# Kernel optimization log

Measured on AMD Instinct MI355X. Metric: run time of the kernel, lower is better.

The kernel has to match this reference:

```python
import jax, jax.numpy as jnp
import numpy as np

DIM = 384; HEADS = 12; WS = 7; SHIFT = 3
IMG_H = 56; IMG_W = 56; B = 32; MLP_HID = 1536
N = WS * WS; HEAD_DIM = DIM // HEADS


def _rel_pos_index():
    # standard Swin relative position index, shape [N, N], values in [0, (2*WS-1)^2)
    coords = np.stack(np.meshgrid(np.arange(WS), np.arange(WS), indexing='ij')).reshape(2, -1)
    rel = (coords[:, :, None] - coords[:, None, :]).transpose(1, 2, 0)
    rel[..., 0] += WS - 1
    rel[..., 1] += WS - 1
    rel[..., 0] *= 2 * WS - 1
    return jnp.asarray(rel.sum(-1))

REL_IDX = _rel_pos_index()


def _shift_mask():
    # Swin shifted-window attention mask: 0 within region, -100 across regions
    img = np.zeros((IMG_H, IMG_W))
    cnt = 0
    for hs in (slice(0, -WS), slice(-WS, -SHIFT), slice(-SHIFT, None)):
        for ws_ in (slice(0, -WS), slice(-WS, -SHIFT), slice(-SHIFT, None)):
            img[hs, ws_] = cnt
            cnt += 1
    mw = img.reshape(IMG_H // WS, WS, IMG_W // WS, WS).transpose(0, 2, 1, 3).reshape(-1, N)
    am = mw[:, None, :] - mw[:, :, None]
    return jnp.asarray(np.where(am != 0, -100.0, 0.0).astype(np.float32))


def setup_inputs() -> dict:
    key = jax.random.key(0)
    ks = jax.random.split(key, 8)
    rn = lambda k, s: jax.random.normal(k, s, jnp.float32) * 0.02
    return {
        'x': jax.random.normal(ks[0], (B, IMG_H * IMG_W, DIM), jnp.float32),
        'mask': _shift_mask(),
        'w_ln1': jnp.ones((DIM,), jnp.float32), 'b_ln1': jnp.zeros((DIM,), jnp.float32),
        'w_qkv': rn(ks[1], (3 * DIM, DIM)), 'b_qkv': jnp.zeros((3 * DIM,), jnp.float32),
        'rel_bias': rn(ks[2], ((2 * WS - 1) ** 2, HEADS)),
        'w_proj': rn(ks[3], (DIM, DIM)), 'b_proj': jnp.zeros((DIM,), jnp.float32),
        'w_ln2': jnp.ones((DIM,), jnp.float32), 'b_ln2': jnp.zeros((DIM,), jnp.float32),
        'w_fc1': rn(ks[4], (MLP_HID, DIM)), 'b_fc1': jnp.zeros((MLP_HID,), jnp.float32),
        'w_fc2': rn(ks[5], (DIM, MLP_HID)), 'b_fc2': jnp.zeros((DIM,), jnp.float32),
        'H': IMG_H, 'W': IMG_W,
    }


def _ln(x, g, b, eps=1e-5):
    mu = x.mean(-1, keepdims=True)
    var = ((x - mu) ** 2).mean(-1, keepdims=True)
    return (x - mu) * jax.lax.rsqrt(var + eps) * g + b


def reference(x, mask, w_ln1, b_ln1, w_qkv, b_qkv, rel_bias, w_proj, b_proj,
              w_ln2, b_ln2, w_fc1, b_fc1, w_fc2, b_fc2, H, W):
    Bsz, L, C = x.shape
    nW = (H // WS) * (W // WS)
    shortcut = x
    h = _ln(x, w_ln1, b_ln1).reshape(Bsz, H, W, C)
    # cyclic shift
    h = jnp.roll(h, (-SHIFT, -SHIFT), axis=(1, 2))
    # window partition -> [B*nW, N, C]
    h = h.reshape(Bsz, H // WS, WS, W // WS, WS, C).transpose(0, 1, 3, 2, 4, 5).reshape(-1, N, C)
    nB = h.shape[0]
    qkv = (h @ w_qkv.T + b_qkv).reshape(nB, N, 3, HEADS, HEAD_DIM).transpose(2, 0, 3, 1, 4)
    q, k, v = qkv[0] * (HEAD_DIM ** -0.5), qkv[1], qkv[2]  # each [nB, heads, N, hd]
    attn = jnp.einsum('bhnd,bhmd->bhnm', q, k)
    bias = rel_bias[REL_IDX].transpose(2, 0, 1)  # [heads, N, N]
    attn = attn + bias[None]
    attn = attn.reshape(Bsz, nW, HEADS, N, N) + mask[None, :, None]
    attn = jax.nn.softmax(attn, axis=-1).reshape(nB, HEADS, N, N)
    o = jnp.einsum('bhnm,bhmd->bhnd', attn, v).transpose(0, 2, 1, 3).reshape(nB, N, C)
    o = o @ w_proj.T + b_proj
    # window reverse
    o = o.reshape(Bsz, H // WS, W // WS, WS, WS, C).transpose(0, 1, 3, 2, 4, 5).reshape(Bsz, H, W, C)
    o = jnp.roll(o, (SHIFT, SHIFT), axis=(1, 2)).reshape(Bsz, H * W, C)
    x = shortcut + o
    h2 = _ln(x, w_ln2, b_ln2)
    h2 = jax.nn.gelu(h2 @ w_fc1.T + b_fc1) @ w_fc2.T + b_fc2
    return x + h2
```

## Files before the change

### kernel.cpp

```cpp
#include <hip/hip_runtime.h>
#include <stdint.h>

#define B_     32
#define IMG    56
#define L_     (IMG*IMG)
#define C_     384
#define HEADS_ 12
#define HD     32
#define WS_    7
#define N_     49
#define NWIN   64
#define NB     (B_*NWIN)
#define M_TOK  (NB*N_)
#define QKVF   1152

typedef __attribute__((ext_vector_type(8))) short bf16x8;
typedef __attribute__((ext_vector_type(4))) float f32x4;
typedef __attribute__((ext_vector_type(4))) unsigned short u16x4;

__device__ __forceinline__ float bf2f(unsigned short u) {
  union { unsigned int u; float f; } c; c.u = ((unsigned int)u) << 16; return c.f;
}
__device__ __forceinline__ unsigned short f2bf(float f) {
  union { float f; unsigned int u; } c; c.f = f;
  unsigned int r = c.u + 0x7FFFu + ((c.u >> 16) & 1u);
  return (unsigned short)(r >> 16);
}

__device__ __forceinline__ void gload_lds16(const void* g, void* l) {
  __builtin_amdgcn_global_load_lds(
      (const __attribute__((address_space(1))) unsigned int*)(uintptr_t)g,
      (__attribute__((address_space(3))) unsigned int*)(uintptr_t)l,
      16, 0, 0);
}

#define MFMA16(a, b, c) __builtin_amdgcn_mfma_f32_16x16x32_bf16((a), (b), (c), 0, 0, 0)

__global__ __launch_bounds__(256) void k_f2b(const float* __restrict__ src,
                                             ushort* __restrict__ dst, int n) {
  int i = blockIdx.x * 256 + threadIdx.x;
  if (i < n) dst[i] = f2bf(src[i]);
}

template<bool WINDOW>
__global__ __launch_bounds__(256) void k_ln(const float* __restrict__ X,
    const float* __restrict__ G, const float* __restrict__ Bb,
    ushort* __restrict__ out)
{
  int token = blockIdx.x * 4 + (threadIdx.x >> 6);
  int lane  = threadIdx.x & 63;
  const float* xp = X + (size_t)token * C_;
  float v[6];
#pragma unroll
  for (int t = 0; t < 6; t++) v[t] = xp[lane + 64*t];
  float s = 0.f, s2 = 0.f;
#pragma unroll
  for (int t = 0; t < 6; t++) { s += v[t]; s2 += v[t]*v[t]; }
#pragma unroll
  for (int off = 32; off > 0; off >>= 1) {
    s  += __shfl_down(s,  off, 64);
    s2 += __shfl_down(s2, off, 64);
  }
  s = __shfl(s, 0, 64); s2 = __shfl(s2, 0, 64);
  float mu   = s * (1.f / C_);
  float rstd = rsqrtf(s2 * (1.f / C_) - mu * mu + 1e-5f);
  size_t obase;
  if (WINDOW) {
    int b = token / L_, pix = token % L_;
    int hi = pix / IMG, wj = pix % IMG;
    int sh = hi - 3; if (sh < 0) sh += IMG;
    int sw = wj - 3; if (sw < 0) sw += IMG;
    int w = b * NWIN + (sh / WS_) * 8 + (sw / WS_);
    int p = (sh % WS_) * WS_ + (sw % WS_);
    obase = ((size_t)w * N_ + p) * C_;
  } else {
    obase = (size_t)token * C_;
  }
#pragma unroll
  for (int t = 0; t < 6; t++) {
    int c = lane + 64*t;
    out[obase + c] = f2bf((v[t] - mu) * rstd * G[c] + Bb[c]);
  }
}

template<int EPI, typename OutT>
__global__ __launch_bounds__(256, 2) void k_gemm(
    const ushort* __restrict__ A, const ushort* __restrict__ W,
    const float* __restrict__ bias, OutT* __restrict__ out,
    const float* __restrict__ res, int M, int N, int K)
{
  __shared__ __align__(16) ushort As[128*32];
  __shared__ __align__(16) ushort Bs[128*32];
  int ntn = N >> 7;
  int m0 = (blockIdx.x / ntn) << 7;
  int n0 = (blockIdx.x % ntn) << 7;
  int tid  = threadIdx.x;
  int wave = tid >> 6, lane = tid & 63;
  int l15  = lane & 15, quad = lane >> 4;
  int wm = (wave & 1) << 6, wn = (wave >> 1) << 6;

  int srow0 = wave * 32 + (lane >> 2);
  int srow1 = srow0 + 16;
  int scol  = (lane & 3) * 8;
  const ushort* gA0 = A + (size_t)(m0 + srow0) * K + scol;
  const ushort* gA1 = A + (size_t)(m0 + srow1) * K + scol;
  const ushort* gB0 = W + (size_t)(n0 + srow0) * K + scol;
  const ushort* gB1 = W + (size_t)(n0 + srow1) * K + scol;
  ushort* lA0 = &As[srow0 * 32 + scol];
  ushort* lA1 = &As[srow1 * 32 + scol];
  ushort* lB0 = &Bs[srow0 * 32 + scol];
  ushort* lB1 = &Bs[srow1 * 32 + scol];

  f32x4 acc[4][4];
#pragma unroll
  for (int i = 0; i < 4; i++)
#pragma unroll
    for (int j = 0; j < 4; j++) acc[i][j] = (f32x4){0.f, 0.f, 0.f, 0.f};

  for (int k0 = 0; k0 < K; k0 += 32) {
    gload_lds16(gA0, lA0);
    gload_lds16(gA1, lA1);
    gload_lds16(gB0, lB0);
    gload_lds16(gB1, lB1);
    gA0 += 32; gA1 += 32; gB0 += 32; gB1 += 32;
    asm volatile("s_waitcnt vmcnt(0)" : : : "memory");
    __syncthreads();
    bf16x8 af[4], bfr[4];
#pragma unroll
    for (int i = 0; i < 4; i++) af[i]  = *(const bf16x8*)&As[(wm + i*16 + l15)*32 + quad*8];
#pragma unroll
    for (int j = 0; j < 4; j++) bfr[j] = *(const bf16x8*)&Bs[(wn + j*16 + l15)*32 + quad*8];
#pragma unroll
    for (int i = 0; i < 4; i++)
#pragma unroll
      for (int j = 0; j < 4; j++)
        acc[i][j] = MFMA16(af[i], bfr[j], acc[i][j]);
    __syncthreads();
  }

  float bv[4];
#pragma unroll
  for (int j = 0; j < 4; j++) bv[j] = bias[n0 + wn + j*16 + l15];
#pragma unroll
  for (int i = 0; i < 4; i++) {
#pragma unroll
    for (int r = 0; r < 4; r++) {
      int row = m0 + wm + i*16 + quad*4 + r;
      size_t dstbase;
      if (EPI == 1) {
        int w = row / N_, p = row % N_;
        int b = w >> 6, wi = w & 63;
        int hi = (wi >> 3) * WS_ + p / WS_ + 3; if (hi >= IMG) hi -= IMG;
        int wj = (wi & 7)  * WS_ + p % WS_ + 3; if (wj >= IMG) wj -= IMG;
        dstbase = ((size_t)b * L_ + hi * IMG + wj) * C_;
      } else {
        dstbase = (size_t)row * N;
      }
#pragma unroll
      for (int j = 0; j < 4; j++) {
        int col = n0 + wn + j*16 + l15;
        float v = acc[i][j][r] + bv[j];
        if (EPI == 2) {
          float x3 = v * v * v;
          v = 0.5f * v * (1.f + tanhf(0.7978845608028654f * (v + 0.044715f * x3)));
        }
        size_t dst = dstbase + col;
        if (EPI == 1) v += res[dst];
        if (EPI == 3) v += res[(size_t)row * N + col];
        if constexpr (sizeof(OutT) == 4) out[dst] = v;
        else                             out[dst] = f2bf(v);
      }
    }
  }
}

__global__ __launch_bounds__(256) void k_bm(const float* __restrict__ relb,
    const float* __restrict__ mask, ushort* __restrict__ bm)
{
  int n = blockIdx.x * 256 + threadIdx.x;
  int r    = n & 3;
  int col  = (n >> 2) & 63;
  int quad = (n >> 8) & 3;
  int i    = (n >> 10) & 3;
  int hw   = n >> 12;
  int h = hw % HEADS_, wc = hw / HEADS_;
  int row = i * 16 + quad * 4 + r;
  float v;
  if (col >= N_) v = -30000.f;
  else if (row >= N_) v = 0.f;
  else {
    int idx = (row / WS_ - col / WS_ + 6) * 13 + (row % WS_ - col % WS_ + 6);
    v = relb[idx * HEADS_ + h] + mask[((size_t)wc * N_ + row) * N_ + col];
  }
  bm[n] = f2bf(v);
}

__global__ __launch_bounds__(256, 3) void k_attn_mfma(
    const ushort* __restrict__ qkv, const ushort* __restrict__ bm,
    ushort* __restrict__ out)
{
  __shared__ __align__(16) ushort Ps[4][64*64];
  __shared__ __align__(16) ushort Vt[4][32*64];
  int wave = threadIdx.x >> 6, lane = threadIdx.x & 63;
  int task = blockIdx.x * 4 + wave;
  int w = task / HEADS_, h = task % HEADS_;
  int l15 = lane & 15, quad = lane >> 4;

  const ushort* base = qkv + (size_t)w * N_ * QKVF + h * HD;

  bf16x8 qf[4], kf[4];
#pragma unroll
  for (int i = 0; i < 4; i++) {
    int rr = i * 16 + l15; if (rr > 48) rr = 48;
    const ushort* rp = base + (size_t)rr * QKVF + quad * 8;
    qf[i] = *(const bf16x8*)rp;
    kf[i] = *(const bf16x8*)(rp + C_);
  }

  {
    int m = lane > 48 ? 48 : lane;
    const ushort* vp = base + (size_t)m * QKVF + 2 * C_;
    bf16x8 v0 = *(const bf16x8*)vp;
    bf16x8 v1 = *(const bf16x8*)(vp + 8);
    bf16x8 v2 = *(const bf16x8*)(vp + 16);
    bf16x8 v3 = *(const bf16x8*)(vp + 24);
    ushort* vt = &Vt[wave][0];
#pragma unroll
    for (int d = 0; d < 32; d++) {
      ushort val = (ushort)(d < 8 ? v0[d & 7] : d < 16 ? v1[d & 7]
                                  : d < 24 ? v2[d & 7] : v3[d & 7]);
      vt[d * 64 + (lane ^ ((d & 7) << 3))] = val;
    }
  }

  f32x4 acc[4][4];
#pragma unroll
  for (int i = 0; i < 4; i++)
#pragma unroll
    for (int j = 0; j < 4; j++) acc[i][j] = (f32x4){0.f, 0.f, 0.f, 0.f};
#pragma unroll
  for (int i = 0; i < 4; i++)
#pragma unroll
    for (int j = 0; j < 4; j++)
      acc[i][j] = MFMA16(qf[i], kf[j], acc[i][j]);

  const ushort* bmb = bm + ((size_t)(w & 63) * HEADS_ + h) * 4096;
  float sv[4][4][4];
#pragma unroll
  for (int i = 0; i < 4; i++)
#pragma unroll
    for (int j = 0; j < 4; j++) {
      u16x4 bv = *(const u16x4*)(bmb + (((i * 4 + quad) * 64) + (j * 16 + l15)) * 4);
#pragma unroll
      for (int r = 0; r < 4; r++)
        sv[i][j][r] = acc[i][j][r] * 0.17677669529663687f + bf2f(bv[r]);
    }

  float mx[4][4], sm[4][4];
#pragma unroll
  for (int i = 0; i < 4; i++)
#pragma unroll
    for (int r = 0; r < 4; r++)
      mx[i][r] = fmaxf(fmaxf(sv[i][0][r], sv[i][1][r]),
                       fmaxf(sv[i][2][r], sv[i][3][r]));
#pragma unroll
  for (int off = 1; off <= 8; off <<= 1)
#pragma unroll
    for (int i = 0; i < 4; i++)
#pragma unroll
      for (int r = 0; r < 4; r++)
        mx[i][r] = fmaxf(mx[i][r], __shfl_xor(mx[i][r], off, 64));
#pragma unroll
  for (int i = 0; i < 4; i++)
#pragma unroll
    for (int r = 0; r < 4; r++) sm[i][r] = 0.f;
#pragma unroll
  for (int i = 0; i < 4; i++)
#pragma unroll
    for (int j = 0; j < 4; j++)
#pragma unroll
      for (int r = 0; r < 4; r++) {
        float e = __expf(sv[i][j][r] - mx[i][r]);
        sv[i][j][r] = e;
        sm[i][r] += e;
      }
#pragma unroll
  for (int off = 1; off <= 8; off <<= 1)
#pragma unroll
    for (int i = 0; i < 4; i++)
#pragma unroll
      for (int r = 0; r < 4; r++)
        sm[i][r] += __shfl_xor(sm[i][r], off, 64);

  ushort* pw = &Ps[wave][0];
#pragma unroll
  for (int i = 0; i < 4; i++)
#pragma unroll
    for (int r = 0; r < 4; r++) {
      float inv = 1.f / sm[i][r];
      int row = i * 16 + quad * 4 + r;
      int s = (row & 7) << 3;
#pragma unroll
      for (int j = 0; j < 4; j++)
        pw[row * 64 + ((j * 16 + l15) ^ s)] = f2bf(sv[i][j][r] * inv);
    }

  f32x4 o[4][2];
#pragma unroll
  for (int i = 0; i < 4; i++)
#pragma unroll
    for (int jv = 0; jv < 2; jv++) o[i][jv] = (f32x4){0.f, 0.f, 0.f, 0.f};
  const ushort* vt = &Vt[wave][0];
#pragma unroll
  for (int ks = 0; ks < 2; ks++) {
    int kc = ks * 32 + quad * 8;
    bf16x8 pa[4], vb[2];
#pragma unroll
    for (int i = 0; i < 4; i++) {
      int row = i * 16 + l15;
      pa[i] = *(const bf16x8*)&pw[row * 64 + (kc ^ ((row & 7) << 3))];
    }
#pragma unroll
    for (int jv = 0; jv < 2; jv++) {
      int nn = jv * 16 + l15;
      vb[jv] = *(const bf16x8*)&vt[nn * 64 + (kc ^ ((nn & 7) << 3))];
    }
#pragma unroll
    for (int i = 0; i < 4; i++)
#pragma unroll
      for (int jv = 0; jv < 2; jv++)
        o[i][jv] = MFMA16(pa[i], vb[jv], o[i][jv]);
  }

  ushort* op = out + ((size_t)w * N_) * C_ + h * HD;
#pragma unroll
  for (int i = 0; i < 4; i++)
#pragma unroll
    for (int r = 0; r < 4; r++) {
      int row = i * 16 + quad * 4 + r;
      if (row < N_) {
#pragma unroll
        for (int jv = 0; jv < 2; jv++)
          op[(size_t)row * C_ + jv * 16 + l15] = f2bf(o[i][jv][r]);
      }
    }
}

extern "C" void kernel_launch(void* const* d_in, const int* in_sizes, int n_in,
                              void* d_out, int out_size, void* d_ws, size_t ws_size,
                              hipStream_t stream) {
  (void)in_sizes; (void)n_in; (void)out_size; (void)ws_size;
  const float* x      = (const float*)d_in[0];
  const float* mask   = (const float*)d_in[1];
  const float* w_ln1  = (const float*)d_in[2];
  const float* b_ln1  = (const float*)d_in[3];
  const float* w_qkv  = (const float*)d_in[4];
  const float* b_qkv  = (const float*)d_in[5];
  const float* relb   = (const float*)d_in[6];
  const float* w_proj = (const float*)d_in[7];
  const float* b_proj = (const float*)d_in[8];
  const float* w_ln2  = (const float*)d_in[9];
  const float* b_ln2  = (const float*)d_in[10];
  const float* w_fc1  = (const float*)d_in[11];
  const float* b_fc1  = (const float*)d_in[12];
  const float* w_fc2  = (const float*)d_in[13];
  const float* b_fc2  = (const float*)d_in[14];

  char* ws = (char*)d_ws;
  ushort* r0 = (ushort*)ws;
  ushort* r1 = (ushort*)(ws + 308281344);
  ushort* bmt = (ushort*)(ws + 231211008);
  ushort* wbq = (ushort*)(ws + 385351680);
  ushort* wbp = wbq + QKVF * C_;
  ushort* wb1 = wbp + C_ * C_;
  ushort* wb2 = wb1 + 1536 * C_;
  float*  x1   = (float*)d_out;
  float*  outp = (float*)d_out;

  k_f2b<<<(QKVF*C_ + 255)/256, 256, 0, stream>>>(w_qkv,  wbq, QKVF*C_);
  k_f2b<<<(C_*C_   + 255)/256, 256, 0, stream>>>(w_proj, wbp, C_*C_);
  k_f2b<<<(1536*C_ + 255)/256, 256, 0, stream>>>(w_fc1,  wb1, 1536*C_);
  k_f2b<<<(C_*1536 + 255)/256, 256, 0, stream>>>(w_fc2,  wb2, C_*1536);
  k_bm<<<(NWIN*HEADS_*4096)/256, 256, 0, stream>>>(relb, mask, bmt);

  k_ln<true ><<<M_TOK/4, 256, 0, stream>>>(x, w_ln1, b_ln1, r1);
  k_gemm<0, ushort><<<(M_TOK/128)*(QKVF/128), 256, 0, stream>>>(
      r1, wbq, b_qkv, r0, nullptr, M_TOK, QKVF, 384);
  k_attn_mfma<<<NB*HEADS_/4, 256, 0, stream>>>(r0, bmt, r1);
  k_gemm<1, float><<<(M_TOK/128)*(C_/128), 256, 0, stream>>>(
      r1, wbp, b_proj, x1, x, M_TOK, C_, 384);
  k_ln<false><<<M_TOK/4, 256, 0, stream>>>(x1, w_ln2, b_ln2, r1);
  k_gemm<2, ushort><<<(M_TOK/128)*(1536/128), 256, 0, stream>>>(
      r1, wb1, b_fc1, r0, nullptr, M_TOK, 1536, 384);
  k_gemm<3, float><<<(M_TOK/128)*(C_/128), 256, 0, stream>>>(
      r0, wb2, b_fc2, outp, x1, M_TOK, C_, 1536);
}
```

Measured before the change: 1.137 ms.

## Double-buffer GEMM LDS tiles, remap block order, use exp-based GELU

The GEMM kernel now double-buffers its A and B shared-memory tiles, so global-to-LDS loads for the next K step are issued before the MFMAs on the current tile. This replaces the serial load, wait, compute pattern. Block indices are also remapped in an interleaved stride-8 order, which changes which output tiles run at the same time and so the cache locality. The tanh GELU is rewritten as the equivalent sigmoid form using __expf, which lowers epilogue cost. LDS use doubles, which may limit occupancy at the two-blocks-per-CU launch bound. The remap assumes the grid size is divisible by 8.

New measurement: 1.056 ms. 7.1% less time.

```diff
diff --git a/kernel.cpp b/kernel.cpp
--- a/kernel.cpp
+++ b/kernel.cpp
@@ -89,11 +89,13 @@
     const float* __restrict__ bias, OutT* __restrict__ out,
     const float* __restrict__ res, int M, int N, int K)
 {
-  __shared__ __align__(16) ushort As[128*32];
-  __shared__ __align__(16) ushort Bs[128*32];
+  __shared__ __align__(16) ushort As[2][128*32];
+  __shared__ __align__(16) ushort Bs[2][128*32];
   int ntn = N >> 7;
-  int m0 = (blockIdx.x / ntn) << 7;
-  int n0 = (blockIdx.x % ntn) << 7;
+  int nwg = gridDim.x;
+  int bid = (blockIdx.x & 7) * (nwg >> 3) + (blockIdx.x >> 3);
+  int m0 = (bid / ntn) << 7;
+  int n0 = (bid % ntn) << 7;
   int tid  = threadIdx.x;
   int wave = tid >> 6, lane = tid & 63;
   int l15  = lane & 15, quad = lane >> 4;
@@ -106,10 +108,8 @@
   const ushort* gA1 = A + (size_t)(m0 + srow1) * K + scol;
   const ushort* gB0 = W + (size_t)(n0 + srow0) * K + scol;
   const ushort* gB1 = W + (size_t)(n0 + srow1) * K + scol;
-  ushort* lA0 = &As[srow0 * 32 + scol];
-  ushort* lA1 = &As[srow1 * 32 + scol];
-  ushort* lB0 = &Bs[srow0 * 32 + scol];
-  ushort* lB1 = &Bs[srow1 * 32 + scol];
+  int oA0 = srow0 * 32 + scol;
+  int oA1 = srow1 * 32 + scol;
 
   f32x4 acc[4][4];
 #pragma unroll
@@ -117,25 +117,38 @@
 #pragma unroll
     for (int j = 0; j < 4; j++) acc[i][j] = (f32x4){0.f, 0.f, 0.f, 0.f};
 
-  for (int k0 = 0; k0 < K; k0 += 32) {
-    gload_lds16(gA0, lA0);
-    gload_lds16(gA1, lA1);
-    gload_lds16(gB0, lB0);
-    gload_lds16(gB1, lB1);
-    gA0 += 32; gA1 += 32; gB0 += 32; gB1 += 32;
+  gload_lds16(gA0, &As[0][oA0]);
+  gload_lds16(gA1, &As[0][oA1]);
+  gload_lds16(gB0, &Bs[0][oA0]);
+  gload_lds16(gB1, &Bs[0][oA1]);
+  gA0 += 32; gA1 += 32; gB0 += 32; gB1 += 32;
+  asm volatile("s_waitcnt vmcnt(0)" : : : "memory");
+  __syncthreads();
+
+  int nt = K >> 5;
+  int cur = 0;
+  for (int t = 0; t < nt; t++) {
+    int nxt = cur ^ 1;
+    if (t + 1 < nt) {
+      gload_lds16(gA0, &As[nxt][oA0]);
+      gload_lds16(gA1, &As[nxt][oA1]);
+      gload_lds16(gB0, &Bs[nxt][oA0]);
+      gload_lds16(gB1, &Bs[nxt][oA1]);
+      gA0 += 32; gA1 += 32; gB0 += 32; gB1 += 32;
+    }
+    bf16x8 af[4], bfr[4];
+#pragma unroll
+    for (int i = 0; i < 4; i++) af[i]  = *(const bf16x8*)&As[cur][(wm + i*16 + l15)*32 + quad*8];
+#pragma unroll
+    for (int j = 0; j < 4; j++) bfr[j] = *(const bf16x8*)&Bs[cur][(wn + j*16 + l15)*32 + quad*8];
+#pragma unroll
+    for (int i = 0; i < 4; i++)
+#pragma unroll
+      for (int j = 0; j < 4; j++)
+        acc[i][j] = MFMA16(af[i], bfr[j], acc[i][j]);
     asm volatile("s_waitcnt vmcnt(0)" : : : "memory");
     __syncthreads();
-    bf16x8 af[4], bfr[4];
-#pragma unroll
-    for (int i = 0; i < 4; i++) af[i]  = *(const bf16x8*)&As[(wm + i*16 + l15)*32 + quad*8];
-#pragma unroll
-    for (int j = 0; j < 4; j++) bfr[j] = *(const bf16x8*)&Bs[(wn + j*16 + l15)*32 + quad*8];
-#pragma unroll
-    for (int i = 0; i < 4; i++)
-#pragma unroll
-      for (int j = 0; j < 4; j++)
-        acc[i][j] = MFMA16(af[i], bfr[j], acc[i][j]);
-    __syncthreads();
+    cur = nxt;
   }
 
   float bv[4];
@@ -161,8 +174,7 @@
         int col = n0 + wn + j*16 + l15;
         float v = acc[i][j][r] + bv[j];
         if (EPI == 2) {
-          float x3 = v * v * v;
-          v = 0.5f * v * (1.f + tanhf(0.7978845608028654f * (v + 0.044715f * x3)));
+          v = v / (1.f + __expf(-1.5957691216057308f * (v + 0.044715f * v * v * v)));
         }
         size_t dst = dstbase + col;
         if (EPI == 1) v += res[dst];
```

## Rewrite GEMM with 256x128 tiles, A fragments straight from global, swizzled LDS B

Applied to the files above, without the earlier changes.

Replaces the 128x128 LDS-tiled GEMM with a 256x128 tile per workgroup. A fragments are loaded directly from global into registers and double-buffered. Only the weight tile is staged in LDS, 128-wide along K, with an XOR swizzle to avoid bank conflicts. It also remaps block indices in an interleaved order to improve L2 locality, and rewrites the tanh-GELU as an algebraically equivalent sigmoid using __expf. The aim is to cut LDS traffic and barriers per MFMA and raise arithmetic intensity. The cost is higher register pressure (32 accumulators per thread) and uncoalesced direct global A loads.

After: 1.322 ms. 1.16x slower.

```diff
diff --git a/kernel.cpp b/kernel.cpp
--- a/kernel.cpp
+++ b/kernel.cpp
@@ -83,64 +83,88 @@
   }
 }
 
-template<int EPI, typename OutT>
-__global__ __launch_bounds__(256, 2) void k_gemm(
+template<int EPI, typename OutT, int K>
+__global__ __launch_bounds__(256, 2) void k_gemm2(
     const ushort* __restrict__ A, const ushort* __restrict__ W,
     const float* __restrict__ bias, OutT* __restrict__ out,
-    const float* __restrict__ res, int M, int N, int K)
+    const float* __restrict__ res, int M, int N)
 {
-  __shared__ __align__(16) ushort As[128*32];
-  __shared__ __align__(16) ushort Bs[128*32];
+  __shared__ __align__(16) ushort Bs[128*128];
+  constexpr int NCH = K / 128;
   int ntn = N >> 7;
-  int m0 = (blockIdx.x / ntn) << 7;
-  int n0 = (blockIdx.x % ntn) << 7;
+  int nwg = gridDim.x;
+  int bid = (blockIdx.x & 7) * (nwg >> 3) + (blockIdx.x >> 3);
+  int m0 = (bid / ntn) << 8;
+  int n0 = (bid % ntn) << 7;
   int tid  = threadIdx.x;
   int wave = tid >> 6, lane = tid & 63;
   int l15  = lane & 15, quad = lane >> 4;
-  int wm = (wave & 1) << 6, wn = (wave >> 1) << 6;
-
-  int srow0 = wave * 32 + (lane >> 2);
-  int srow1 = srow0 + 16;
-  int scol  = (lane & 3) * 8;
-  const ushort* gA0 = A + (size_t)(m0 + srow0) * K + scol;
-  const ushort* gA1 = A + (size_t)(m0 + srow1) * K + scol;
-  const ushort* gB0 = W + (size_t)(n0 + srow0) * K + scol;
-  const ushort* gB1 = W + (size_t)(n0 + srow1) * K + scol;
-  ushort* lA0 = &As[srow0 * 32 + scol];
-  ushort* lA1 = &As[srow1 * 32 + scol];
-  ushort* lB0 = &Bs[srow0 * 32 + scol];
-  ushort* lB1 = &Bs[srow1 * 32 + scol];
-
-  f32x4 acc[4][4];
-#pragma unroll
-  for (int i = 0; i < 4; i++)
-#pragma unroll
-    for (int j = 0; j < 4; j++) acc[i][j] = (f32x4){0.f, 0.f, 0.f, 0.f};
-
-  for (int k0 = 0; k0 < K; k0 += 32) {
-    gload_lds16(gA0, lA0);
-    gload_lds16(gA1, lA1);
-    gload_lds16(gB0, lB0);
-    gload_lds16(gB1, lB1);
-    gA0 += 32; gA1 += 32; gB0 += 32; gB1 += 32;
-    asm volatile("s_waitcnt vmcnt(0)" : : : "memory");
-    __syncthreads();
-    bf16x8 af[4], bfr[4];
-#pragma unroll
-    for (int i = 0; i < 4; i++) af[i]  = *(const bf16x8*)&As[(wm + i*16 + l15)*32 + quad*8];
-#pragma unroll
-    for (int j = 0; j < 4; j++) bfr[j] = *(const bf16x8*)&Bs[(wn + j*16 + l15)*32 + quad*8];
-#pragma unroll
-    for (int i = 0; i < 4; i++)
-#pragma unroll
-      for (int j = 0; j < 4; j++)
-        acc[i][j] = MFMA16(af[i], bfr[j], acc[i][j]);
-    __syncthreads();
-  }
-
-  float bv[4];
-#pragma unroll
-  for (int j = 0; j < 4; j++) bv[j] = bias[n0 + wn + j*16 + l15];
+  int wm = wave << 6;
+
+  int srow = (wave << 2) + (lane >> 4);
+  int scg  = l15 ^ (srow & 7);
+  const ushort* gB = W + (size_t)(n0 + srow) * K + scg * 8;
+  ushort* lB = &Bs[srow * 128 + l15 * 8];
+
+  const ushort* gA = A + (size_t)(m0 + wm + l15) * K + quad * 8;
+
+  f32x4 acc[4][8];
+#pragma unroll
+  for (int i = 0; i < 4; i++)
+#pragma unroll
+    for (int j = 0; j < 8; j++) acc[i][j] = (f32x4){0.f, 0.f, 0.f, 0.f};
+
+#pragma unroll
+  for (int it = 0; it < 8; it++)
+    gload_lds16(gB + (size_t)it * 16 * K, lB + it * 2048);
+  bf16x8 afc[4], afn[4];
+#pragma unroll
+  for (int i = 0; i < 4; i++)
+    afc[i] = *(const bf16x8*)(gA + (size_t)i * 16 * K);
+  asm volatile("s_waitcnt vmcnt(0)" ::: "memory");
+  __builtin_amdgcn_s_barrier();
+
+  const ushort* gAn = gA + 32;
+  const ushort* gBk = gB;
+
+  for (int ch = 0; ch < NCH; ch++) {
+#pragma unroll
+    for (int ss = 0; ss < 4; ss++) {
+      bool last = (ch == NCH - 1) && (ss == 3);
+      if (!last) {
+#pragma unroll
+        for (int i = 0; i < 4; i++)
+          afn[i] = *(const bf16x8*)(gAn + (size_t)i * 16 * K);
+        gAn += 32;
+      }
+#pragma unroll
+      for (int j = 0; j < 8; j++) {
+        int row = j * 16 + l15;
+        int cg  = (ss * 4 + quad) ^ (row & 7);
+        bf16x8 b = *(const bf16x8*)&Bs[row * 128 + cg * 8];
+#pragma unroll
+        for (int i = 0; i < 4; i++)
+          acc[i][j] = MFMA16(afc[i], b, acc[i][j]);
+      }
+      if (ss == 3 && ch + 1 < NCH) {
+        __builtin_amdgcn_s_barrier();
+        gBk += 128;
+#pragma unroll
+        for (int it = 0; it < 8; it++)
+          gload_lds16(gBk + (size_t)it * 16 * K, lB + it * 2048);
+        asm volatile("s_waitcnt vmcnt(0)" ::: "memory");
+        __builtin_amdgcn_s_barrier();
+      }
+      if (!last) {
+#pragma unroll
+        for (int i = 0; i < 4; i++) afc[i] = afn[i];
+      }
+    }
+  }
+
+  float bv[8];
+#pragma unroll
+  for (int j = 0; j < 8; j++) bv[j] = bias[n0 + j*16 + l15];
 #pragma unroll
   for (int i = 0; i < 4; i++) {
 #pragma unroll
@@ -157,12 +181,11 @@
         dstbase = (size_t)row * N;
       }
 #pragma unroll
-      for (int j = 0; j < 4; j++) {
-        int col = n0 + wn + j*16 + l15;
+      for (int j = 0; j < 8; j++) {
+        int col = n0 + j*16 + l15;
         float v = acc[i][j][r] + bv[j];
         if (EPI == 2) {
-          float x3 = v * v * v;
-          v = 0.5f * v * (1.f + tanhf(0.7978845608028654f * (v + 0.044715f * x3)));
+          v = v / (1.f + __expf(-1.5957691216057308f * (v + 0.044715f * v * v * v)));
         }
         size_t dst = dstbase + col;
         if (EPI == 1) v += res[dst];
@@ -384,14 +407,14 @@
   k_bm<<<(NWIN*HEADS_*4096)/256, 256, 0, stream>>>(relb, mask, bmt);
 
   k_ln<true ><<<M_TOK/4, 256, 0, stream>>>(x, w_ln1, b_ln1, r1);
-  k_gemm<0, ushort><<<(M_TOK/128)*(QKVF/128), 256, 0, stream>>>(
-      r1, wbq, b_qkv, r0, nullptr, M_TOK, QKVF, 384);
+  k_gemm2<0, ushort, 384><<<(M_TOK/256)*(QKVF/128), 256, 0, stream>>>(
+      r1, wbq, b_qkv, r0, nullptr, M_TOK, QKVF);
   k_attn_mfma<<<NB*HEADS_/4, 256, 0, stream>>>(r0, bmt, r1);
-  k_gemm<1, float><<<(M_TOK/128)*(C_/128), 256, 0, stream>>>(
-      r1, wbp, b_proj, x1, x, M_TOK, C_, 384);
+  k_gemm2<1, float, 384><<<(M_TOK/256)*(C_/128), 256, 0, stream>>>(
+      r1, wbp, b_proj, x1, x, M_TOK, C_);
   k_ln<false><<<M_TOK/4, 256, 0, stream>>>(x1, w_ln2, b_ln2, r1);
-  k_gemm<2, ushort><<<(M_TOK/128)*(1536/128), 256, 0, stream>>>(
-      r1, wb1, b_fc1, r0, nullptr, M_TOK, 1536, 384);
-  k_gemm<3, float><<<(M_TOK/128)*(C_/128), 256, 0, stream>>>(
-      r0, wb2, b_fc2, outp, x1, M_TOK, C_, 1536);
-}
+  k_gemm2<2, ushort, 384><<<(M_TOK/256)*(1536/128), 256, 0, stream>>>(
+      r1, wb1, b_fc1, r0, nullptr, M_TOK, 1536);
+  k_gemm2<3, float, 1536><<<(M_TOK/256)*(C_/128), 256, 0, stream>>>(
+      r0, wb2, b_fc2, outp, x1, M_TOK, C_);
+}
```
